# Kernel optimization log

Measured on AMD Instinct MI355X. Metric: run time of the kernel, lower is better.

Reference implementation:

```python
import jax, jax.numpy as jnp
import numpy as np

N, D, V = 4096, 512, 50000
K = 10  # accuracy_slack_size


def setup_inputs() -> dict:
    key = jax.random.key(0)
    k1, k2, k3, k4 = jax.random.split(key, 4)
    logits = jax.random.normal(k1, (N, D), dtype=jnp.float32)
    target = jax.random.randint(k2, (N,), 0, V, dtype=jnp.int64)
    mask = jax.random.randint(k3, (N,), 0, 2, dtype=jnp.int32)
    word_vectors = jax.random.normal(k4, (V, D), dtype=jnp.float32)
    return {"logits": logits, "target": target, "mask": mask, "word_vectors": word_vectors}


def reference(logits, target, mask, word_vectors):
    # Brute-force euclidean kNN: squared distances suffice for neighbor ranking.
    # d2[n, v] = ||x_n||^2 - 2 x_n . w_v + ||w_v||^2   -> [N, V]
    x2 = jnp.sum(logits * logits, axis=-1, keepdims=True)          # [N, 1]
    w2 = jnp.sum(word_vectors * word_vectors, axis=-1)             # [V]
    d2 = x2 - 2.0 * (logits @ word_vectors.T) + w2[None, :]        # [N, V]
    # top-K smallest distances -> indices of K nearest words
    _, words = jax.lax.top_k(-d2, K)                               # [N, K]
    # membership check: is the target word among the K neighbors
    hit = jnp.any(words == target[:, None], axis=-1)               # [N] bool
    m = mask.astype(jnp.float32)
    acc = jnp.sum(m * hit.astype(jnp.float32)) / jnp.sum(m)
    return jnp.reshape(acc, (1,))
```

## Files before the change

kernel.cpp:

```cpp
#include <hip/hip_runtime.h>
#include <stdint.h>

#define N_ROWS 4096
#define DIM    512
#define VOCAB  50000
#define VPAD   50048
#define TOPK   10
#define MARGIN 8.0f
#define ECHUNKS 196

typedef int   i32x4 __attribute__((ext_vector_type(4)));
typedef float f32x4 __attribute__((ext_vector_type(4)));

#define GLOBAL_AS __attribute__((address_space(1)))
#define LDS_AS    __attribute__((address_space(3)))

__device__ __forceinline__ void quant_row(const float* __restrict__ src,
                                          signed char* __restrict__ dst,
                                          int lane, float* rowmax_out,
                                          float* w2_out) {
    const float4* s4 = (const float4*)(src + lane * 8);
    float4 a = s4[0], b = s4[1];
    float mx = fmaxf(fmaxf(fmaxf(fabsf(a.x), fabsf(a.y)), fmaxf(fabsf(a.z), fabsf(a.w))),
                     fmaxf(fmaxf(fabsf(b.x), fabsf(b.y)), fmaxf(fabsf(b.z), fabsf(b.w))));
    float w2 = a.x*a.x + a.y*a.y + a.z*a.z + a.w*a.w
             + b.x*b.x + b.y*b.y + b.z*b.z + b.w*b.w;
    #pragma unroll
    for (int off = 1; off < 64; off <<= 1) {
        mx  = fmaxf(mx, __shfl_xor(mx, off, 64));
        w2 += __shfl_xor(w2, off, 64);
    }
    float inv = 127.0f / fmaxf(mx, 1e-30f);
    int q0 = (int)rintf(a.x * inv), q1 = (int)rintf(a.y * inv);
    int q2 = (int)rintf(a.z * inv), q3 = (int)rintf(a.w * inv);
    int q4 = (int)rintf(b.x * inv), q5 = (int)rintf(b.y * inv);
    int q6 = (int)rintf(b.z * inv), q7 = (int)rintf(b.w * inv);
    uint2 pk;
    pk.x = (q0 & 0xff) | ((q1 & 0xff) << 8) | ((q2 & 0xff) << 16) | ((unsigned)(q3 & 0xff) << 24);
    pk.y = (q4 & 0xff) | ((q5 & 0xff) << 8) | ((q6 & 0xff) << 16) | ((unsigned)(q7 & 0xff) << 24);
    *(uint2*)(dst + lane * 8) = pk;
    *rowmax_out = mx;
    *w2_out = w2;
}

__global__ __launch_bounds__(256) void quantize_x(const float* __restrict__ X,
                                                  signed char* __restrict__ Xq,
                                                  float* __restrict__ sx) {
    int wave = threadIdx.x >> 6, lane = threadIdx.x & 63;
    int row = blockIdx.x * 4 + wave;
    float mx, w2;
    quant_row(X + (size_t)row * DIM, Xq + (size_t)row * DIM, lane, &mx, &w2);
    if (lane == 0) sx[row] = fmaxf(mx, 1e-30f) / 127.0f;
}

__global__ __launch_bounds__(256) void quantize_w(const float* __restrict__ W,
                                                  signed char* __restrict__ Wq,
                                                  float* __restrict__ sw,
                                                  float* __restrict__ w2) {
    int wave = threadIdx.x >> 6, lane = threadIdx.x & 63;
    int row = blockIdx.x * 4 + wave;
    if (row < VOCAB) {
        float mx, s2;
        quant_row(W + (size_t)row * DIM, Wq + (size_t)row * DIM, lane, &mx, &s2);
        if (lane == 0) { sw[row] = fmaxf(mx, 1e-30f) / 127.0f; w2[row] = s2; }
    } else {
        *(uint2*)(Wq + (size_t)row * DIM + lane * 8) = make_uint2(0, 0);
        if (lane == 0) { sw[row] = 0.0f; w2[row] = 1e30f; }
    }
}

__global__ __launch_bounds__(64) void st_kernel(const float* __restrict__ X,
                                                const float* __restrict__ W,
                                                const int* __restrict__ target,
                                                float* __restrict__ st) {
    int n = blockIdx.x;
    int t = target[n];
    const float4* x4 = (const float4*)(X + (size_t)n * DIM);
    const float4* w4 = (const float4*)(W + (size_t)t * DIM);
    int lane = threadIdx.x;
    float4 xa = x4[lane], xb = x4[lane + 64];
    float4 wa = w4[lane], wb = w4[lane + 64];
    float sxw = xa.x*wa.x + xa.y*wa.y + xa.z*wa.z + xa.w*wa.w
              + xb.x*wb.x + xb.y*wb.y + xb.z*wb.z + xb.w*wb.w;
    float sww = wa.x*wa.x + wa.y*wa.y + wa.z*wa.z + wa.w*wa.w
              + wb.x*wb.x + wb.y*wb.y + wb.z*wb.z + wb.w*wb.w;
    #pragma unroll
    for (int off = 32; off > 0; off >>= 1) {
        sxw += __shfl_down(sxw, off, 64);
        sww += __shfl_down(sww, off, 64);
    }
    if (lane == 0) st[n] = sww - 2.0f * sxw;
}

__global__ __launch_bounds__(256) void count_mfma_i8(
        const signed char* __restrict__ Xq, const signed char* __restrict__ Wq,
        const float* __restrict__ sx, const float* __restrict__ sw,
        const float* __restrict__ w2, const float* __restrict__ st,
        const int* __restrict__ target,
        int* __restrict__ cnt_def, int* __restrict__ cnt_unc) {

    __shared__ signed char Als[128 * 64];
    __shared__ signed char Bls[128 * 64];
    __shared__ float w2_s[128];
    __shared__ float sw_s[128];
    __shared__ float st_s[128];
    __shared__ float sx_s[128];
    __shared__ int   t_s[128];
    __shared__ int   pk_s[128];

    const int tid  = threadIdx.x;
    const int wave = tid >> 6, lane = tid & 63;
    const int row0 = blockIdx.x * 128;
    const int col0 = blockIdx.y * 128;

    if (tid < 128) { w2_s[tid] = w2[col0 + tid]; sw_s[tid] = sw[col0 + tid]; pk_s[tid] = 0; }
    else           { st_s[tid - 128] = st[row0 + tid - 128];
                     sx_s[tid - 128] = sx[row0 + tid - 128];
                     t_s[tid - 128]  = target[row0 + tid - 128]; }

    const signed char* ga = Xq + (size_t)(row0 + wave*32 + (lane >> 2)) * DIM + (lane & 3) * 16;
    const signed char* gb = Wq + (size_t)(col0 + wave*32 + (lane >> 2)) * DIM + (lane & 3) * 16;
    signed char* la0 = &Als[(wave*32     ) * 64];
    signed char* la1 = &Als[(wave*32 + 16) * 64];
    signed char* lb0 = &Bls[(wave*32     ) * 64];
    signed char* lb1 = &Bls[(wave*32 + 16) * 64];

    const int q = lane >> 4, c = lane & 15;
    const int wm = wave >> 1, wn = wave & 1;
    const signed char* ap = &Als[(wm*64 + c) * 64 + q * 16];
    const signed char* bp = &Bls[(wn*64 + c) * 64 + q * 16];

    i32x4 acc[4][4];
    #pragma unroll
    for (int i = 0; i < 4; i++)
        #pragma unroll
        for (int j = 0; j < 4; j++) acc[i][j] = (i32x4){0, 0, 0, 0};

    for (int k0 = 0; k0 < DIM; k0 += 64) {
        __builtin_amdgcn_global_load_lds((const GLOBAL_AS void*)(ga + k0),           (LDS_AS void*)la0, 16, 0, 0);
        __builtin_amdgcn_global_load_lds((const GLOBAL_AS void*)(ga + 16*DIM + k0),  (LDS_AS void*)la1, 16, 0, 0);
        __builtin_amdgcn_global_load_lds((const GLOBAL_AS void*)(gb + k0),           (LDS_AS void*)lb0, 16, 0, 0);
        __builtin_amdgcn_global_load_lds((const GLOBAL_AS void*)(gb + 16*DIM + k0),  (LDS_AS void*)lb1, 16, 0, 0);
        __syncthreads();
        i32x4 af[4], bfr[4];
        #pragma unroll
        for (int i = 0; i < 4; i++) af[i]  = *(const i32x4*)(ap + i * 16 * 64);
        #pragma unroll
        for (int j = 0; j < 4; j++) bfr[j] = *(const i32x4*)(bp + j * 16 * 64);
        #pragma unroll
        for (int i = 0; i < 4; i++)
            #pragma unroll
            for (int j = 0; j < 4; j++)
                acc[i][j] = __builtin_amdgcn_mfma_i32_16x16x64_i8(af[i], bfr[j], acc[i][j], 0, 0, 0);
        __syncthreads();
    }

    #pragma unroll
    for (int i = 0; i < 4; i++) {
        #pragma unroll
        for (int reg = 0; reg < 4; reg++) {
            int r = wm*64 + i*16 + q*4 + reg;
            float stv = st_s[r];
            float sxr = sx_s[r];
            int   t   = t_s[r];
            int def = 0, unc = 0;
            #pragma unroll
            for (int j = 0; j < 4; j++) {
                int col_l = wn*64 + j*16 + c;
                float dot = sxr * sw_s[col_l] * (float)acc[i][j][reg];
                float s = w2_s[col_l] - 2.0f * dot;
                int v = col0 + col_l;
                if (v != t) {
                    if      (s < stv - MARGIN) def++;
                    else if (s < stv + MARGIN) unc++;
                }
            }
            int pk = (def << 16) | unc;
            pk += __shfl_xor(pk, 1, 64);
            pk += __shfl_xor(pk, 2, 64);
            pk += __shfl_xor(pk, 4, 64);
            pk += __shfl_xor(pk, 8, 64);
            if (c == 0) atomicAdd(&pk_s[r], pk);
        }
    }
    __syncthreads();
    if (tid < 128) {
        int pk = pk_s[tid];
        if (pk) {
            atomicAdd(&cnt_def[row0 + tid], pk >> 16);
            atomicAdd(&cnt_unc[row0 + tid], pk & 0xffff);
        }
    }
}

__global__ __launch_bounds__(256) void resolve_kernel(const int* __restrict__ cnt_def,
                                                      const int* __restrict__ cnt_unc,
                                                      int* __restrict__ hit,
                                                      int* __restrict__ amb_rows,
                                                      int* __restrict__ amb_count) {
    int n = blockIdx.x * 256 + threadIdx.x;
    if (n >= N_ROWS) return;
    int d = cnt_def[n], u = cnt_unc[n];
    int h;
    if (d >= TOPK) h = 0;
    else if (d + u < TOPK) h = 1;
    else { int idx = atomicAdd(amb_count, 1); amb_rows[idx] = n; h = 2; }
    hit[n] = h;
}

__global__ __launch_bounds__(256) void exact_kernel(const float* __restrict__ X,
                                                    const float* __restrict__ W,
                                                    const float* __restrict__ w2,
                                                    const float* __restrict__ st,
                                                    const int* __restrict__ target,
                                                    const int* __restrict__ amb_rows,
                                                    const int* __restrict__ amb_count,
                                                    int* __restrict__ count_exact) {
    __shared__ float xs[DIM];
    __shared__ int scnt[4];
    const int tid = threadIdx.x, wave = tid >> 6, lane = tid & 63;
    const int nw = amb_count[0] * ECHUNKS;
    for (int w = blockIdx.x; w < nw; w += gridDim.x) {
        const int row   = amb_rows[w / ECHUNKS];
        const int chunk = w % ECHUNKS;
        __syncthreads();
        for (int i = tid; i < DIM; i += 256) xs[i] = X[(size_t)row * DIM + i];
        if (tid < 4) scnt[tid] = 0;
        __syncthreads();
        const float4 xa = *(const float4*)&xs[lane * 8];
        const float4 xb = *(const float4*)&xs[lane * 8 + 4];
        const float stv = st[row];
        const int   t   = target[row];
        int cnt = 0;
        const int v0 = chunk * 256 + wave * 64;
        #pragma unroll 2
        for (int i = 0; i < 64; i++) {
            int v = v0 + i;
            if (v < VOCAB) {
                const float4* wr = (const float4*)(W + (size_t)v * DIM + lane * 8);
                float4 wa = wr[0], wb = wr[1];
                float p = xa.x*wa.x + xa.y*wa.y + xa.z*wa.z + xa.w*wa.w
                        + xb.x*wb.x + xb.y*wb.y + xb.z*wb.z + xb.w*wb.w;
                p += __shfl_xor(p, 1, 64);
                p += __shfl_xor(p, 2, 64);
                p += __shfl_xor(p, 4, 64);
                p += __shfl_xor(p, 8, 64);
                p += __shfl_xor(p, 16, 64);
                p += __shfl_xor(p, 32, 64);
                float s = w2[v] - 2.0f * p;
                if (lane == 0 && v != t && (s < stv || (s == stv && v < t))) cnt++;
            }
        }
        if (lane == 0) scnt[wave] = cnt;
        __syncthreads();
        if (tid == 0)
            atomicAdd(&count_exact[row], scnt[0] + scnt[1] + scnt[2] + scnt[3]);
    }
}

__global__ __launch_bounds__(256) void finalize2(const int* __restrict__ hit,
                                                 const int* __restrict__ count_exact,
                                                 const int* __restrict__ mask,
                                                 float* __restrict__ out) {
    int tid = threadIdx.x;
    int hits = 0, msum = 0;
    for (int n = tid; n < N_ROWS; n += 256) {
        int m = mask[n];
        msum += m;
        int h = hit[n];
        int hv = (h == 2) ? (count_exact[n] < TOPK ? 1 : 0) : h;
        if (m) hits += hv;
    }
    #pragma unroll
    for (int off = 32; off > 0; off >>= 1) {
        hits += __shfl_down(hits, off, 64);
        msum += __shfl_down(msum, off, 64);
    }
    __shared__ int sh[8];
    int wid = tid >> 6, lane = tid & 63;
    if (lane == 0) { sh[wid] = hits; sh[4 + wid] = msum; }
    __syncthreads();
    if (tid == 0) {
        int H = sh[0] + sh[1] + sh[2] + sh[3];
        int M = sh[4] + sh[5] + sh[6] + sh[7];
        out[0] = (float)H / (float)M;
    }
}

#define BM 128
#define BN 128
#define BK 16
#define TM 8
#define TN 8

__global__ __launch_bounds__(64) void w2_kernel_fb(const float* __restrict__ W,
                                                   float* __restrict__ w2) {
    int v = blockIdx.x;
    const float4* w4 = (const float4*)(W + (size_t)v * DIM);
    int lane = threadIdx.x;
    float4 a = w4[lane];
    float4 b = w4[lane + 64];
    float s = a.x*a.x + a.y*a.y + a.z*a.z + a.w*a.w
            + b.x*b.x + b.y*b.y + b.z*b.z + b.w*b.w;
    #pragma unroll
    for (int off = 32; off > 0; off >>= 1) s += __shfl_down(s, off, 64);
    if (lane == 0) w2[v] = s;
}

__global__ __launch_bounds__(256) void count_kernel_fb(
        const float* __restrict__ X, const float* __restrict__ W,
        const float* __restrict__ w2, const float* __restrict__ st,
        const int* __restrict__ target, int* __restrict__ count) {
    __shared__ float Xs[BK][BM];
    __shared__ float Ws[BK][BN];
    __shared__ float st_s[BM];
    __shared__ int   t_s[BM];
    __shared__ float w2_s[BN];
    const int tid  = threadIdx.x;
    const int row0 = blockIdx.y * BM;
    const int col0 = blockIdx.x * BN;
    if (tid < 128) { st_s[tid] = st[row0 + tid]; t_s[tid] = target[row0 + tid]; }
    else { int cc = tid - 128; int v = col0 + cc; if (v >= VOCAB) v = VOCAB - 1; w2_s[cc] = w2[v]; }
    float acc[TM][TN] = {};
    const int tx = tid & 15;
    const int ty = tid >> 4;
    for (int k0 = 0; k0 < DIM; k0 += BK) {
        #pragma unroll
        for (int j = 0; j < 2; j++) {
            int idx = tid + 256 * j;
            int r   = idx >> 2;
            int kq  = idx & 3;
            float4 xv = *(const float4*)(X + (size_t)(row0 + r) * DIM + k0 + kq * 4);
            Xs[kq*4+0][r] = xv.x; Xs[kq*4+1][r] = xv.y;
            Xs[kq*4+2][r] = xv.z; Xs[kq*4+3][r] = xv.w;
            int v = col0 + r; if (v >= VOCAB) v = VOCAB - 1;
            float4 wv = *(const float4*)(W + (size_t)v * DIM + k0 + kq * 4);
            Ws[kq*4+0][r] = wv.x; Ws[kq*4+1][r] = wv.y;
            Ws[kq*4+2][r] = wv.z; Ws[kq*4+3][r] = wv.w;
        }
        __syncthreads();
        #pragma unroll
        for (int kk = 0; kk < BK; kk++) {
            float a[TM], b[TN];
            #pragma unroll
            for (int i = 0; i < TM; i++) a[i] = Xs[kk][ty * TM + i];
            #pragma unroll
            for (int j = 0; j < TN; j++) b[j] = Ws[kk][tx * TN + j];
            #pragma unroll
            for (int i = 0; i < TM; i++)
                #pragma unroll
                for (int j = 0; j < TN; j++)
                    acc[i][j] += a[i] * b[j];
        }
        __syncthreads();
    }
    int cnt[TM];
    #pragma unroll
    for (int i = 0; i < TM; i++) {
        cnt[i] = 0;
        float stv = st_s[ty * TM + i];
        int   t   = t_s[ty * TM + i];
        #pragma unroll
        for (int j = 0; j < TN; j++) {
            int v = col0 + tx * TN + j;
            float s = w2_s[tx * TN + j] - 2.0f * acc[i][j];
            if (v < VOCAB && v != t && (s < stv || (s == stv && v < t))) cnt[i]++;
        }
    }
    __syncthreads();
    int* scnt = (int*)Xs;
    #pragma unroll
    for (int i = 0; i < TM; i++) scnt[(ty * TM + i) * 16 + tx] = cnt[i];
    __syncthreads();
    if (tid < BM) {
        int s = 0;
        #pragma unroll
        for (int j = 0; j < 16; j++) s += scnt[tid * 16 + j];
        atomicAdd(&count[row0 + tid], s);
    }
}

__global__ __launch_bounds__(256) void finalize_fb(const int* __restrict__ count,
                                                   const int* __restrict__ mask,
                                                   float* __restrict__ out) {
    int tid = threadIdx.x;
    int hits = 0, msum = 0;
    for (int n = tid; n < N_ROWS; n += 256) {
        int m = mask[n];
        msum += m;
        if (m && count[n] < TOPK) hits++;
    }
    #pragma unroll
    for (int off = 32; off > 0; off >>= 1) {
        hits += __shfl_down(hits, off, 64);
        msum += __shfl_down(msum, off, 64);
    }
    __shared__ int sh[8];
    int wid = tid >> 6, lane = tid & 63;
    if (lane == 0) { sh[wid] = hits; sh[4 + wid] = msum; }
    __syncthreads();
    if (tid == 0) {
        int H = sh[0] + sh[1] + sh[2] + sh[3];
        int M = sh[4] + sh[5] + sh[6] + sh[7];
        out[0] = (float)H / (float)M;
    }
}

extern "C" void kernel_launch(void* const* d_in, const int* in_sizes, int n_in,
                              void* d_out, int out_size, void* d_ws, size_t ws_size,
                              hipStream_t stream) {
    const float* X      = (const float*)d_in[0];
    const int*   target = (const int*)d_in[1];
    const int*   mask   = (const int*)d_in[2];
    const float* W      = (const float*)d_in[3];
    float* out = (float*)d_out;
    char* ws = (char*)d_ws;

    const size_t oXq   = 0;
    const size_t oWq   = oXq  + (size_t)N_ROWS * DIM;
    const size_t osx   = oWq  + (size_t)VPAD  * DIM;
    const size_t osw   = osx  + (size_t)N_ROWS * 4;
    const size_t ow2   = osw  + (size_t)VPAD * 4;
    const size_t ost   = ow2  + (size_t)VPAD * 4;
    const size_t ocd   = ost  + (size_t)N_ROWS * 4;
    const size_t ocu   = ocd  + (size_t)N_ROWS * 4;
    const size_t oce   = ocu  + (size_t)N_ROWS * 4;
    const size_t ohit  = oce  + (size_t)N_ROWS * 4;
    const size_t oamb  = ohit + (size_t)N_ROWS * 4;
    const size_t oambc = oamb + (size_t)N_ROWS * 4;
    const size_t need  = oambc + 16;

    if (ws_size >= need) {
        signed char* Xq = (signed char*)(ws + oXq);
        signed char* Wq = (signed char*)(ws + oWq);
        float* sx = (float*)(ws + osx);
        float* sw = (float*)(ws + osw);
        float* w2 = (float*)(ws + ow2);
        float* st = (float*)(ws + ost);
        int* cnt_def = (int*)(ws + ocd);
        int* cnt_unc = (int*)(ws + ocu);
        int* count_exact = (int*)(ws + oce);
        int* hit = (int*)(ws + ohit);
        int* amb_rows = (int*)(ws + oamb);
        int* amb_count = (int*)(ws + oambc);

        hipMemsetAsync(ws + ocd, 0, oambc + 16 - ocd, stream);
        quantize_x<<<N_ROWS / 4, 256, 0, stream>>>(X, Xq, sx);
        quantize_w<<<VPAD / 4, 256, 0, stream>>>(W, Wq, sw, w2);
        st_kernel<<<N_ROWS, 64, 0, stream>>>(X, W, target, st);
        count_mfma_i8<<<dim3(N_ROWS / 128, VPAD / 128), 256, 0, stream>>>(
            Xq, Wq, sx, sw, w2, st, target, cnt_def, cnt_unc);
        resolve_kernel<<<16, 256, 0, stream>>>(cnt_def, cnt_unc, hit, amb_rows, amb_count);
        exact_kernel<<<2048, 256, 0, stream>>>(X, W, w2, st, target, amb_rows, amb_count, count_exact);
        finalize2<<<1, 256, 0, stream>>>(hit, count_exact, mask, out);
    } else {
        float* w2 = (float*)ws;
        float* st = (float*)(ws + 200704);
        int* countp = (int*)(ws + 200704 + 16384);
        hipMemsetAsync(countp, 0, N_ROWS * sizeof(int), stream);
        w2_kernel_fb<<<VOCAB, 64, 0, stream>>>(W, w2);
        st_kernel<<<N_ROWS, 64, 0, stream>>>(X, W, target, st);
        dim3 grid((VOCAB + BN - 1) / BN, N_ROWS / BM);
        count_kernel_fb<<<grid, 256, 0, stream>>>(X, W, w2, st, target, countp);
        finalize_fb<<<1, 256, 0, stream>>>(countp, mask, out);
    }
}
```

Baseline: 457.9 us.

## Rescan ambiguous rows with int8 band filter and verify only band pairs exactly

Rows the int8 MFMA pass cannot classify were previously rescanned in full FP32 against the whole vocabulary. Now a band_rescan kernel recomputes the int8 distance for each ambiguous row and vocab pair and collects only the candidates inside the uncertainty margin. An exact_pairs kernel then checks those few pairs in FP32, starting from the definite count. Rows with more than 64 band candidates fall back to the full exact scan. This cuts the FP32 work, but adds one wave per (row, vocab) pair plus heavy atomics, which could be costly if many rows are ambiguous.

```diff
diff --git a/kernel.cpp b/kernel.cpp
--- a/kernel.cpp
+++ b/kernel.cpp
@@ -7,10 +7,10 @@
 #define VPAD   50048
 #define TOPK   10
 #define MARGIN 8.0f
+#define MAXB   64
 #define ECHUNKS 196
 
 typedef int   i32x4 __attribute__((ext_vector_type(4)));
-typedef float f32x4 __attribute__((ext_vector_type(4)));
 
 #define GLOBAL_AS __attribute__((address_space(1)))
 #define LDS_AS    __attribute__((address_space(3)))
@@ -196,6 +196,7 @@
 __global__ __launch_bounds__(256) void resolve_kernel(const int* __restrict__ cnt_def,
                                                       const int* __restrict__ cnt_unc,
                                                       int* __restrict__ hit,
+                                                      int* __restrict__ count_exact,
                                                       int* __restrict__ amb_rows,
                                                       int* __restrict__ amb_count) {
     int n = blockIdx.x * 256 + threadIdx.x;
@@ -204,8 +205,102 @@
     int h;
     if (d >= TOPK) h = 0;
     else if (d + u < TOPK) h = 1;
-    else { int idx = atomicAdd(amb_count, 1); amb_rows[idx] = n; h = 2; }
+    else {
+        h = 2;
+        count_exact[n] = d;
+        int idx = atomicAdd(amb_count, 1);
+        amb_rows[idx] = n;
+    }
     hit[n] = h;
+}
+
+__device__ __forceinline__ int dot4i8(int a, int b, int acc) {
+#if __has_builtin(__builtin_amdgcn_sdot4)
+    return __builtin_amdgcn_sdot4(a, b, acc, false);
+#else
+    #pragma unroll
+    for (int j = 0; j < 4; j++)
+        acc += (int)(signed char)(a >> (8*j)) * (int)(signed char)(b >> (8*j));
+    return acc;
+#endif
+}
+
+__global__ __launch_bounds__(256) void band_rescan(
+        const signed char* __restrict__ Xq, const signed char* __restrict__ Wq,
+        const float* __restrict__ sx, const float* __restrict__ sw,
+        const float* __restrict__ w2, const float* __restrict__ st,
+        const int* __restrict__ target,
+        const int* __restrict__ amb_rows, const int* __restrict__ amb_count,
+        int* __restrict__ band_n, unsigned int* __restrict__ pairs,
+        int* __restrict__ pair_count,
+        int* __restrict__ full_rows, int* __restrict__ full_count,
+        int* __restrict__ ov) {
+    const int wave = threadIdx.x >> 6, lane = threadIdx.x & 63;
+    const long ntask = (long)amb_count[0] * VPAD;
+    for (long idx = (long)blockIdx.x * 4 + wave; idx < ntask; idx += (long)gridDim.x * 4) {
+        const int row = amb_rows[(int)(idx / VPAD)];
+        const int v   = (int)(idx % VPAD);
+        int2 xa = *(const int2*)(Xq + (size_t)row * DIM + lane * 8);
+        int2 wa = *(const int2*)(Wq + (size_t)v   * DIM + lane * 8);
+        int acc = dot4i8(xa.x, wa.x, 0);
+        acc = dot4i8(xa.y, wa.y, acc);
+        acc += __shfl_xor(acc, 1, 64);
+        acc += __shfl_xor(acc, 2, 64);
+        acc += __shfl_xor(acc, 4, 64);
+        acc += __shfl_xor(acc, 8, 64);
+        acc += __shfl_xor(acc, 16, 64);
+        acc += __shfl_xor(acc, 32, 64);
+        if (lane == 0 && v != target[row]) {
+            float dot = sx[row] * sw[v] * (float)acc;
+            float s = w2[v] - 2.0f * dot;
+            float stv = st[row];
+            if (!(s < stv - MARGIN) && (s < stv + MARGIN)) {
+                int pos = atomicAdd(&band_n[row], 1);
+                if (pos < MAXB) {
+                    int slot = atomicAdd(pair_count, 1);
+                    pairs[slot] = ((unsigned)row << 16) | (unsigned)v;
+                } else if (pos == MAXB) {
+                    int fslot = atomicAdd(full_count, 1);
+                    full_rows[fslot] = row;
+                    ov[row] = 1;
+                }
+            }
+        }
+    }
+}
+
+__global__ __launch_bounds__(256) void exact_pairs(const float* __restrict__ X,
+                                                   const float* __restrict__ W,
+                                                   const float* __restrict__ w2,
+                                                   const float* __restrict__ st,
+                                                   const int* __restrict__ target,
+                                                   const unsigned int* __restrict__ pairs,
+                                                   const int* __restrict__ pair_count,
+                                                   int* __restrict__ count_exact) {
+    const int wave = threadIdx.x >> 6, lane = threadIdx.x & 63;
+    const int np = pair_count[0];
+    for (int p = blockIdx.x * 4 + wave; p < np; p += gridDim.x * 4) {
+        unsigned pk = pairs[p];
+        int row = pk >> 16, v = pk & 0xffff;
+        const float4* xr = (const float4*)(X + (size_t)row * DIM + lane * 8);
+        const float4* wr = (const float4*)(W + (size_t)v   * DIM + lane * 8);
+        float4 xa = xr[0], xb = xr[1];
+        float4 wa = wr[0], wb = wr[1];
+        float pdot = xa.x*wa.x + xa.y*wa.y + xa.z*wa.z + xa.w*wa.w
+                   + xb.x*wb.x + xb.y*wb.y + xb.z*wb.z + xb.w*wb.w;
+        pdot += __shfl_xor(pdot, 1, 64);
+        pdot += __shfl_xor(pdot, 2, 64);
+        pdot += __shfl_xor(pdot, 4, 64);
+        pdot += __shfl_xor(pdot, 8, 64);
+        pdot += __shfl_xor(pdot, 16, 64);
+        pdot += __shfl_xor(pdot, 32, 64);
+        if (lane == 0) {
+            float s = w2[v] - 2.0f * pdot;
+            float stv = st[row];
+            int t = target[row];
+            if (s < stv || (s == stv && v < t)) atomicAdd(&count_exact[row], 1);
+        }
+    }
 }
 
 __global__ __launch_bounds__(256) void exact_kernel(const float* __restrict__ X,
@@ -213,15 +308,15 @@
                                                     const float* __restrict__ w2,
                                                     const float* __restrict__ st,
                                                     const int* __restrict__ target,
-                                                    const int* __restrict__ amb_rows,
-                                                    const int* __restrict__ amb_count,
-                                                    int* __restrict__ count_exact) {
+                                                    const int* __restrict__ full_rows,
+                                                    const int* __restrict__ full_count,
+                                                    int* __restrict__ count_full) {
     __shared__ float xs[DIM];
     __shared__ int scnt[4];
     const int tid = threadIdx.x, wave = tid >> 6, lane = tid & 63;
-    const int nw = amb_count[0] * ECHUNKS;
+    const int nw = full_count[0] * ECHUNKS;
     for (int w = blockIdx.x; w < nw; w += gridDim.x) {
-        const int row   = amb_rows[w / ECHUNKS];
+        const int row   = full_rows[w / ECHUNKS];
         const int chunk = w % ECHUNKS;
         __syncthreads();
         for (int i = tid; i < DIM; i += 256) xs[i] = X[(size_t)row * DIM + i];
@@ -254,12 +349,14 @@
         if (lane == 0) scnt[wave] = cnt;
         __syncthreads();
         if (tid == 0)
-            atomicAdd(&count_exact[row], scnt[0] + scnt[1] + scnt[2] + scnt[3]);
+            atomicAdd(&count_full[row], scnt[0] + scnt[1] + scnt[2] + scnt[3]);
     }
 }
 
 __global__ __launch_bounds__(256) void finalize2(const int* __restrict__ hit,
                                                  const int* __restrict__ count_exact,
+                                                 const int* __restrict__ count_full,
+                                                 const int* __restrict__ ov,
                                                  const int* __restrict__ mask,
                                                  float* __restrict__ out) {
     int tid = threadIdx.x;
@@ -268,7 +365,10 @@
         int m = mask[n];
         msum += m;
         int h = hit[n];
-        int hv = (h == 2) ? (count_exact[n] < TOPK ? 1 : 0) : h;
+        int hv;
+        if (h < 2) hv = h;
+        else if (ov[n]) hv = (count_full[n] < TOPK) ? 1 : 0;
+        else hv = (count_exact[n] < TOPK) ? 1 : 0;
         if (m) hits += hv;
     }
     #pragma unroll
@@ -425,10 +525,15 @@
     const size_t ocd   = ost  + (size_t)N_ROWS * 4;
     const size_t ocu   = ocd  + (size_t)N_ROWS * 4;
     const size_t oce   = ocu  + (size_t)N_ROWS * 4;
-    const size_t ohit  = oce  + (size_t)N_ROWS * 4;
+    const size_t ocf   = oce  + (size_t)N_ROWS * 4;
+    const size_t oov   = ocf  + (size_t)N_ROWS * 4;
+    const size_t obn   = oov  + (size_t)N_ROWS * 4;
+    const size_t ohit  = obn  + (size_t)N_ROWS * 4;
     const size_t oamb  = ohit + (size_t)N_ROWS * 4;
-    const size_t oambc = oamb + (size_t)N_ROWS * 4;
-    const size_t need  = oambc + 16;
+    const size_t ofr   = oamb + (size_t)N_ROWS * 4;
+    const size_t octr  = ofr  + (size_t)N_ROWS * 4;
+    const size_t oprs  = octr + 64;
+    const size_t need  = oprs + (size_t)N_ROWS * MAXB * 4;
 
     if (ws_size >= need) {
         signed char* Xq = (signed char*)(ws + oXq);
@@ -440,19 +545,31 @@
         int* cnt_def = (int*)(ws + ocd);
         int* cnt_unc = (int*)(ws + ocu);
         int* count_exact = (int*)(ws + oce);
+        int* count_full = (int*)(ws + ocf);
+        int* ov = (int*)(ws + oov);
+        int* band_n = (int*)(ws + obn);
         int* hit = (int*)(ws + ohit);
         int* amb_rows = (int*)(ws + oamb);
-        int* amb_count = (int*)(ws + oambc);
-
-        hipMemsetAsync(ws + ocd, 0, oambc + 16 - ocd, stream);
+        int* full_rows = (int*)(ws + ofr);
+        int* amb_count  = (int*)(ws + octr);
+        int* pair_count = (int*)(ws + octr + 16);
+        int* full_count = (int*)(ws + octr + 32);
+        unsigned int* pairs = (unsigned int*)(ws + oprs);
+
+        hipMemsetAsync(ws + ocd, 0, oprs - ocd, stream);
         quantize_x<<<N_ROWS / 4, 256, 0, stream>>>(X, Xq, sx);
         quantize_w<<<VPAD / 4, 256, 0, stream>>>(W, Wq, sw, w2);
         st_kernel<<<N_ROWS, 64, 0, stream>>>(X, W, target, st);
         count_mfma_i8<<<dim3(N_ROWS / 128, VPAD / 128), 256, 0, stream>>>(
             Xq, Wq, sx, sw, w2, st, target, cnt_def, cnt_unc);
-        resolve_kernel<<<16, 256, 0, stream>>>(cnt_def, cnt_unc, hit, amb_rows, amb_count);
-        exact_kernel<<<2048, 256, 0, stream>>>(X, W, w2, st, target, amb_rows, amb_count, count_exact);
-        finalize2<<<1, 256, 0, stream>>>(hit, count_exact, mask, out);
+        resolve_kernel<<<16, 256, 0, stream>>>(cnt_def, cnt_unc, hit, count_exact,
+                                               amb_rows, amb_count);
+        band_rescan<<<512, 256, 0, stream>>>(Xq, Wq, sx, sw, w2, st, target,
+                                             amb_rows, amb_count, band_n,
+                                             pairs, pair_count, full_rows, full_count, ov);
+        exact_pairs<<<128, 256, 0, stream>>>(X, W, w2, st, target, pairs, pair_count, count_exact);
+        exact_kernel<<<512, 256, 0, stream>>>(X, W, w2, st, target, full_rows, full_count, count_full);
+        finalize2<<<1, 256, 0, stream>>>(hit, count_exact, count_full, ov, mask, out);
     } else {
         float* w2 = (float*)ws;
         float* st = (float*)(ws + 200704);
```

Result: no change. 453.6 us (-0.9%).
